# Optimization experiments

Hardware: AMD Instinct MI355X
Metric: run time of the kernel (lower is better)

## Reference

```python
import jax, jax.numpy as jnp
import numpy as np

NX, NY = 512, 512
FNUM, GNUM = 120, 120
NA = 1.35
WAVELENGTH = NX * NA / 100.0  # chosen so normalized period = 100
N_LIQUID = 1.44
M_RED = 0.25
LOW_LIGHT_THRES = 1e-3
SRC_STEEP = 8.0
RESIST_STEEP = 30.0
RESIST_INT = 0.225
DOSES = (0.98, 1.0, 1.02)
SRC_GRID = 13

X1 = NX // 2 - FNUM; X2 = NX // 2 + FNUM + 1
Y1 = NY // 2 - GNUM; Y2 = NY // 2 + GNUM + 1
_PER_X = NX / (WAVELENGTH / NA)
_PER_Y = NY / (WAVELENGTH / NA)
NORM_SPEC = _PER_X * _PER_Y
DFMDG = 1.0 / NORM_SPEC
_fm = (np.arange(X1, X2) - NX // 2) / _PER_X
_gm = (np.arange(Y1, Y2) - NY // 2) / _PER_Y
_FM, _GM = np.meshgrid(_fm, _gm)  # 'xy' indexing, shape [2*GNUM+1, 2*FNUM+1]
FM = jnp.asarray(_FM, jnp.float32)
GM = jnp.asarray(_GM, jnp.float32)


def cal_pupil(fg2):
    # obliquity factor; pupil phase is identically zero in this module
    num = 1.0 - (M_RED ** 2) * (NA ** 2) * fg2
    den = 1.0 - (NA / N_LIQUID) ** 2 * fg2
    return jnp.sqrt(jnp.sqrt(num / den))


def setup_inputs() -> dict:
    key = jax.random.key(0)
    g = np.linspace(-1.0, 1.0, SRC_GRID, dtype=np.float32)
    fxg, fyg = np.meshgrid(g, g)
    r = np.sqrt(fxg ** 2 + fyg ** 2)
    data = ((r >= 0.6) & (r <= 0.9)).astype(np.float32)  # annular source
    # sigmoid activation init: +1 where lit, -1 elsewhere (zeros, set 2 where data>0.5, sub 1)
    params = 2.0 * data - 1.0
    mask_value = jax.random.uniform(key, (NY, NX), jnp.float32)
    return {
        "mask_value": mask_value,
        "source_params": jnp.asarray(params, jnp.float32),
        "source_fx": jnp.asarray(fxg.reshape(-1), jnp.float32),
        "source_fy": jnp.asarray(fyg.reshape(-1), jnp.float32),
    }


def _forward(mask_value, source_params, source_fx, source_fy):
    # source activation + low-light pruning (masked_select expressed as zero-weighting)
    val = jax.nn.sigmoid(SRC_STEEP * source_params).reshape(-1)  # [S]
    valid = val >= LOW_LIGHT_THRES
    w = jnp.where(valid, val, 0.0)
    weight = jnp.sum(w)

    # normalization intensity (detached in the original)
    fxy2 = source_fx ** 2 + source_fy ** 2
    obl = cal_pupil(jnp.where(valid, fxy2, 0.0))
    norm_I = jax.lax.stop_gradient(
        N_LIQUID * DFMDG ** 2 * jnp.sum(w * (NORM_SPEC * obl) ** 2) / weight
    )

    # shifted pupil per source point over the mask frequency window
    F = FM[None, :, :] + source_fx[:, None, None]  # [S, Gy, Gx]
    G = GM[None, :, :] + source_fy[:, None, None]
    rho2 = F * F + G * G                            # == mask_fg2m + 2(fx*fm+fy*gm) + fxy2
    vmask = rho2 <= 1.0
    pupil = jnp.where(vmask, cal_pupil(jnp.where(vmask, rho2, 0.0)), 0.0)  # [S, Gy, Gx]

    S = w.shape[0]
    Is, Rs = [], []
    for d in DOSES:
        fv = jnp.fft.fftshift(jnp.fft.fft2(jnp.fft.ifftshift(mask_value * d)))
        win = fv[Y1:Y2, X1:X2]                      # [Gy, Gx] complex
        tempH = win[None, :, :] * pupil.astype(jnp.complex64)  # masked spectrum*pupil
        e = jnp.zeros((S, NY, NX), jnp.complex64).at[:, Y1:Y2, X1:X2].set(tempH)
        AA = jnp.fft.fftshift(jnp.fft.ifft2(e), axes=(-2, -1))
        I2 = AA.real ** 2 + AA.imag ** 2            # |AA * conj(AA)|
        intensity = jnp.einsum('s,syx->yx', w, I2) / weight / norm_I
        Is.append(intensity)
        Rs.append(jax.nn.sigmoid(RESIST_STEEP * (intensity - RESIST_INT)))
    # [2, 3, NY, NX]: [0] = aerial intensity per dose, [1] = resist image per dose
    return jnp.stack([jnp.stack(Is), jnp.stack(Rs)])


def reference(mask_value, source_params, source_fx, source_fy):
    return _forward(mask_value, source_params, source_fx, source_fy)
```

## Files before the change

kernel.cpp:

```cpp
#include <hip/hip_runtime.h>
#include <hip/hip_bf16.h>
#include <hip/hip_fp16.h>


#define SPLIT 8

static const size_t O_ACC  = 8192;
static const size_t ACC_BYTES = (size_t)SPLIT * 512 * 512 * 4;
static const size_t O_WIN  = O_ACC + ACC_BYTES;
static const size_t O_R1   = O_WIN + 464896;
static const size_t O_T2   = O_R1 + 987136;
static const size_t SLOT_BYTES = (size_t)512 * 244 * 4;

__device__ inline float2 cadd(float2 a, float2 b){ return make_float2(a.x+b.x, a.y+b.y); }
__device__ inline float2 csub(float2 a, float2 b){ return make_float2(a.x-b.x, a.y-b.y); }
__device__ inline float2 cmul(float2 a, float2 b){
  return make_float2(fmaf(a.x, b.x, -(a.y*b.y)), fmaf(a.x, b.y, a.y*b.x));
}
__device__ inline float2 twsgn(float2 t, int S) {
  return make_float2(t.x, (S > 0) ? t.y : -t.y);
}

__device__ inline void build_twt(float2* twt) {
  for (int k = (int)threadIdx.x; k < 512; k += 256) {
    double a = 6.283185307179586476925286766559 * (double)k / 512.0;
    twt[k] = make_float2((float)cos(a), (float)sin(a));
  }
}

template<int S, bool ZTOP>
__device__ inline void dft8(float2 v[8]) {
  const float sg = (float)S;
  const float C7 = 0.7071067811865476f;
  float2 t0, t1, t2, t3, t4, t5, t6, t7;
  if (ZTOP) {
    t0 = v[0]; t4 = v[0];
    t1 = v[1]; t5 = v[1];
    t2 = v[2]; t6 = v[2];
    t3 = v[3]; t7 = v[3];
  } else {
    t0=cadd(v[0],v[4]); t4=csub(v[0],v[4]);
    t1=cadd(v[1],v[5]); t5=csub(v[1],v[5]);
    t2=cadd(v[2],v[6]); t6=csub(v[2],v[6]);
    t3=cadd(v[3],v[7]); t7=csub(v[3],v[7]);
  }
  t5 = make_float2(C7*(t5.x - sg*t5.y), C7*(t5.y + sg*t5.x));
  t6 = make_float2(-sg*t6.y, sg*t6.x);
  t7 = make_float2(C7*(-t7.x - sg*t7.y), C7*(sg*t7.x - t7.y));
  float2 u0=cadd(t0,t2), u2=csub(t0,t2);
  float2 u1=cadd(t1,t3), u3=csub(t1,t3);
  u3 = make_float2(-sg*u3.y, sg*u3.x);
  float2 u4=cadd(t4,t6), u6=csub(t4,t6);
  float2 u5=cadd(t5,t7), u7=csub(t5,t7);
  u7 = make_float2(-sg*u7.y, sg*u7.x);
  v[0]=cadd(u0,u1); v[4]=csub(u0,u1);
  v[2]=cadd(u2,u3); v[6]=csub(u2,u3);
  v[1]=cadd(u4,u5); v[5]=csub(u4,u5);
  v[3]=cadd(u6,u7); v[7]=csub(u6,u7);
}

template<int S, bool ZTOP>
__device__ inline void wfft512(float2 v[8], int lane, float2* xch,
                               const float2* twt) {
  const int p2 = lane & 7, u0 = lane >> 3;
  dft8<S, ZTOP>(v);
  { float2 t1 = twsgn(twt[lane], S), acc = t1;
    v[1] = cmul(v[1], acc);
    #pragma unroll
    for (int u = 2; u < 8; u++) { acc = cmul(acc, t1); v[u] = cmul(v[u], acc); } }
  __builtin_amdgcn_wave_barrier();
  #pragma unroll
  for (int u = 0; u < 8; u++) xch[u*68 + p2*8 + u0] = v[u];
  __builtin_amdgcn_wave_barrier();
  { const float4* rp = (const float4*)(xch + u0*68 + p2*8);
    #pragma unroll
    for (int q = 0; q < 4; q++) {
      float4 t = rp[q];
      v[2*q]   = make_float2(t.x, t.y);
      v[2*q+1] = make_float2(t.z, t.w);
    } }
  dft8<S, false>(v);
  { float2 t1 = twsgn(twt[p2 << 3], S), acc = t1;
    v[1] = cmul(v[1], acc);
    #pragma unroll
    for (int u = 2; u < 8; u++) { acc = cmul(acc, t1); v[u] = cmul(v[u], acc); } }
  __builtin_amdgcn_wave_barrier();
  #pragma unroll
  for (int u = 0; u < 8; u++) xch[u*68 + lane] = v[u];
  __builtin_amdgcn_wave_barrier();
  { const float4* rp = (const float4*)(xch + p2*68 + u0*8);
    #pragma unroll
    for (int q = 0; q < 4; q++) {
      float4 t = rp[q];
      v[2*q]   = make_float2(t.x, t.y);
      v[2*q+1] = make_float2(t.z, t.w);
    } }
  dft8<S, false>(v);
}

__global__ void __launch_bounds__(256, 6) k_b1(const float* mask, const float* prm,
                                               const float* sfx, const float* sfy,
                                               char* ws, float2* R1t) {
  int t = threadIdx.x, lane = t & 63, wv = t >> 6;
  __shared__ __align__(16) float2 lds[4*544];
  __shared__ __align__(16) float2 twt[512];
  build_twt(twt);
  if (blockIdx.x == 0) {
    float*  sw  = (float*)lds;
    float*  sxx = sw + 192; float* syy = sxx + 192; float* scw = syy + 192;
    double* so  = (double*)(sw + 768);
    int*    skp = (int*)(so + 176);
    if (t < 169) {
      float p = prm[t];
      float val = 1.f / (1.f + __expf(-8.f * p));
      float w = (val >= 0.001f) ? val : 0.f;
      double o = 0.0; float fx = 0.f, fy = 0.f;
      if (w > 0.f) {
        fx = sfx[t]; fy = sfy[t];
        double f2 = (double)fx*(double)fx + (double)fy*(double)fy;
        o = (double)w * sqrt((1.0 - 0.11390625 * f2) / (1.0 - 0.87890625 * f2));
      }
      sw[t] = w; so[t] = o; sxx[t] = fx; syy[t] = fy;
    }
    __syncthreads();
    if (t < 169) {
      float w = sw[t];
      int keep = 0; float cw = w;
      if (w > 0.f) {
        float fx = sxx[t], fy = syy[t];
        int pr = -1;
        for (int s2 = 0; s2 < 169; s2++) {
          if (sw[s2] > 0.f && fabsf(sxx[s2] + fx) < 1e-5f
                           && fabsf(syy[s2] + fy) < 1e-5f) { pr = s2; break; }
        }
        if (pr < 0 || pr == t) keep = 1;
        else if (pr > t) { keep = 1; cw = w + sw[pr]; }
      }
      skp[t] = keep; scw[t] = cw;
    }
    __syncthreads();
    if (t == 0) {
      float* wsf = (float*)ws;
      double Sden = 0.0; int c = 0;
      for (int s = 0; s < 169; s++) {
        Sden += so[s];
        if (skp[s]) { wsf[64+c] = scw[s]; wsf[320+c] = sxx[s]; wsf[576+c] = syy[s]; c++; }
      }
      ((int*)ws)[0] = c;
      wsf[1] = (float)(1.0 / (262144.0 * 1.44 * Sden));
    }
  }
  __syncthreads();
  int y = blockIdx.x * 4 + wv;
  float2 v[8];
  #pragma unroll
  for (int q = 0; q < 8; q++) v[q] = make_float2(mask[y*512 + 64*q + lane], 0.f);
  wfft512<-1, false>(v, lane, lds + wv*544, twt);
  #pragma unroll
  for (int u = 0; u < 8; u++) {
    int k = (lane>>3) + 8*(lane&7) + 64*u;
    int beta = (k >= 392) ? (k - 392) : ((k <= 120) ? (k + 120) : -1);
    if (beta >= 0) R1t[beta*512 + y] = v[u];
  }
}

__global__ void __launch_bounds__(256, 6) k_b2(const float2* R1t, float2* Wg) {
  int lane = threadIdx.x & 63, wv = threadIdx.x >> 6;
  int j = blockIdx.x * 4 + wv;
  __shared__ __align__(16) float2 lds[4*544];
  __shared__ __align__(16) float2 twt[512];
  build_twt(twt);
  __syncthreads();
  float2 v[8];
  #pragma unroll
  for (int q = 0; q < 8; q++)
    v[q] = (j < 241) ? R1t[j*512 + 64*q + lane] : make_float2(0.f, 0.f);
  wfft512<-1, false>(v, lane, lds + wv*544, twt);
  if (j < 241) {
    #pragma unroll
    for (int u = 0; u < 8; u++) {
      int k = (lane>>3) + 8*(lane&7) + 64*u;
      int alpha = (k >= 392) ? (k - 392) : ((k <= 120) ? (k + 120) : -1);
      if (alpha >= 0) Wg[alpha*241 + j] = v[u];
    }
  }
}

__global__ void __launch_bounds__(256, 7) k_c1(const float2* Wg, const char* wsb,
                                               int base, int CH, __half2* T2) {
  const float* wsf = (const float*)wsb;
  __shared__ __align__(16) float2 lds[4*544];
  __shared__ __align__(16) float2 twt[512];
  __shared__ float FMt[241];
  build_twt(twt);
  if (threadIdx.x < 241)
    FMt[threadIdx.x] = (float)(((double)((int)threadIdx.x - 120)) / 100.0);
  __syncthreads();
  int active = *(const int*)wsb - base;
  if (active > CH) active = CH;
  int ntask = active * 31;
  int lane = threadIdx.x & 63, wv = threadIdx.x >> 6;
  float2* xch = lds + wv*544;
  for (int task = (int)blockIdx.x; task < ntask; task += (int)gridDim.x) {
    int sic  = task / 31;
    int tile = task % 31;
    int slot = base + sic;
    float fx = wsf[320 + slot], fy = wsf[576 + slot];
    float sqw = __fsqrt_rn(wsf[64 + slot]) * 0.001953125f;
    #pragma unroll
    for (int ph = 0; ph < 2; ph++) {
      int alpha = tile*8 + ph*4 + wv;
      bool arow = (alpha < 241);
      float Gf = __fadd_rn(arow ? FMt[alpha] : 0.f, fy);
      float g2 = __fmul_rn(Gf, Gf);
      bool active_row = arow && (g2 <= 1.0f);
      float2 v[8];
      #pragma unroll
      for (int q = 0; q < 8; q++) v[q] = make_float2(0.f, 0.f);
      if (active_row) {
        #pragma unroll
        for (int q = 0; q < 4; q++) {
          int n = 64*q + lane;
          if (n < 241) {
            float Ff = __fadd_rn(FMt[n], fx);
            float r2 = __fadd_rn(__fmul_rn(Ff, Ff), g2);
            if (r2 <= 1.0f) {
              float num = fmaf(-0.11390625f, r2, 1.0f);
              float den = fmaf(-0.87890625f, r2, 1.0f);
              float P = __fsqrt_rn(__fsqrt_rn(__fdividef(num, den))) * sqw;
              float2 Wv = Wg[alpha*241 + n];
              v[q] = make_float2(P * Wv.x, P * Wv.y);
            }
          }
        }
        wfft512<1, true>(v, lane, xch, twt);
      }
      #pragma unroll
      for (int u = 0; u < 8; u++) {
        int xx = (lane>>3) + 8*(lane&7) + 64*u;
        xch[xx] = v[u];
      }
      __syncthreads();
      int colb = tile*8 + ph*4;
      if (colb < 244) {
        #pragma unroll
        for (int r = 0; r < 2; r++) {
          int x = (int)threadIdx.x + 256*r;
          union { __half2 h[4]; float4 f; } u;
          #pragma unroll
          for (int wvi = 0; wvi < 4; wvi++) {
            float2 a = lds[wvi*544 + x];
            u.h[wvi] = __floats2half2_rn(a.x, a.y);
          }
          *(float4*)(T2 + ((size_t)sic*512 + x)*244 + colb) = u.f;
        }
      }
      __syncthreads();
    }
  }
}

__global__ void __launch_bounds__(256, 7) k_c2(const __half2* T2, const char* wsb,
                                               int base, int CH, int first,
                                               float* accbuf) {
  const int* cnt = (const int*)wsb;
  int part = blockIdx.x & (SPLIT-1);
  int xg   = blockIdx.x >> 3;
  int lane = threadIdx.x & 63, wv = threadIdx.x >> 6;
  int x = xg*4 + wv;
  __shared__ __align__(16) float2 lds[4*544];
  __shared__ __align__(16) float2 twt[512];
  build_twt(twt);
  __syncthreads();
  float2* xch = lds + wv*544;
  int count = *cnt;
  float av[8] = {0.f,0.f,0.f,0.f,0.f,0.f,0.f,0.f};
  int sic = part;
  bool act = (sic < CH) && (base + sic < count);
  __half2 pv[4] = {{0.f,0.f},{0.f,0.f},{0.f,0.f},{0.f,0.f}};
  if (act) {
    const __half2* row = T2 + ((size_t)sic*512 + x)*244;
    #pragma unroll
    for (int q = 0; q < 4; q++) {
      int n = 64*q + lane;
      pv[q] = (n < 241) ? row[n] : __half2{0.f, 0.f};
    }
  }
  while (act) {
    float2 v[8];
    #pragma unroll
    for (int q = 0; q < 4; q++) { float2 f = __half22float2(pv[q]); v[q] = f; }
    #pragma unroll
    for (int q = 4; q < 8; q++) v[q] = make_float2(0.f, 0.f);
    int nsic = sic + SPLIT;
    act = (nsic < CH) && (base + nsic < count);
    if (act) {
      const __half2* row = T2 + ((size_t)nsic*512 + x)*244;
      #pragma unroll
      for (int q = 0; q < 4; q++) {
        int n = 64*q + lane;
        pv[q] = (n < 241) ? row[n] : __half2{0.f, 0.f};
      }
    }
    wfft512<1, true>(v, lane, xch, twt);
    #pragma unroll
    for (int u = 0; u < 8; u++)
      av[u] += fmaf(v[u].x, v[u].x, v[u].y*v[u].y);
    sic = nsic;
  }
  float* a = accbuf + ((size_t)part << 18) + (size_t)x * 512;
  int y0 = (lane>>3) + 8*(lane&7);
  if (first) {
    #pragma unroll
    for (int u = 0; u < 8; u++) a[y0 + 64*u] = av[u];
  } else {
    #pragma unroll
    for (int u = 0; u < 8; u++) a[y0 + 64*u] += av[u];
  }
}

__global__ void __launch_bounds__(256) k_final(const float* acc, const char* wsb,
                                               float* out) {
  __shared__ float tile[64][65];
  const float* wsf = (const float*)wsb;
  float scale = wsf[1];
  int x0 = (blockIdx.x & 7) * 64, y0 = (blockIdx.x >> 3) * 64;
  int j = threadIdx.x & 63, i0 = threadIdx.x >> 6;
  #pragma unroll
  for (int k = 0; k < 16; k++) {
    int i = i0 + 4*k;
    const float* ap = acc + (size_t)(x0 + i)*512 + y0 + j;
    float s = 0.f;
    #pragma unroll
    for (int p = 0; p < SPLIT; p++) s += ap[(size_t)p << 18];
    tile[i][j] = s;
  }
  __syncthreads();
  const float dd[3] = {0.9604f, 1.0f, 1.0404f};
  #pragma unroll
  for (int k = 0; k < 16; k++) {
    int yy = i0 + 4*k;
    float I = scale * tile[j][yy];
    int o = (y0 + yy)*512 + x0 + j;
    #pragma unroll
    for (int d = 0; d < 3; d++) {
      float Ik = dd[d] * I;
      out[(size_t)d*262144 + o] = Ik;
      out[(size_t)(3+d)*262144 + o] = 1.f / (1.f + __expf(-30.f*(Ik - 0.225f)));
    }
  }
}

extern "C" void kernel_launch(void* const* d_in, const int* in_sizes, int n_in,
                              void* d_out, int out_size, void* d_ws, size_t ws_size,
                              hipStream_t stream) {
  (void)in_sizes; (void)n_in; (void)out_size;
  const float* mask = (const float*)d_in[0];
  const float* prm  = (const float*)d_in[1];
  const float* sfx  = (const float*)d_in[2];
  const float* sfy  = (const float*)d_in[3];
  float* out = (float*)d_out;
  char*  ws  = (char*)d_ws;

  float*   acc = (float*)(ws + O_ACC);
  float2*  Wg  = (float2*)(ws + O_WIN);
  float2*  R1t = (float2*)(ws + O_R1);
  __half2* T2  = (__half2*)(ws + O_T2);

  k_b1<<<dim3(128), dim3(256), 0, stream>>>(mask, prm, sfx, sfy, ws, R1t);
  k_b2<<<dim3(61),  dim3(256), 0, stream>>>(R1t, Wg);

  size_t avail = (ws_size > O_T2) ? (ws_size - O_T2) : 0;
  int CH = (int)(avail / SLOT_BYTES);
  if (CH > 169) CH = 169;
  if (CH < 1)   CH = 1;
  for (int base = 0; base < 169; base += CH) {
    k_c1<<<dim3(1024),      dim3(256), 0, stream>>>(Wg, (const char*)ws, base, CH, T2);
    k_c2<<<dim3(128*SPLIT), dim3(256), 0, stream>>>(T2, (const char*)ws, base, CH,
                                                    (base == 0) ? 1 : 0, acc);
  }
  k_final<<<dim3(64), dim3(256), 0, stream>>>(acc, (const char*)ws, out);
}
```

Before: 139.3 us.

## Fuse all pipeline stages into one cooperative persistent kernel with grid syncs

Merges the row FFT, column FFT, pupil-multiply/inverse-FFT stage, accumulation stage and final normalization into a single cooperative kernel. Stages are separated by grid-wide syncs instead of separate launches. The grid is sized from occupancy queries, and the T2 intermediate layout changes to packed 4-column groups. The change targets launch overhead and per-kernel setup such as twiddle table builds, at the cost of grid-sync latency, lower occupancy (launch bounds 4), and idle blocks in small stages.

New measurement: 349.6 us. +151.0%, slower.

```diff
diff --git a/kernel.cpp b/kernel.cpp
--- a/kernel.cpp
+++ b/kernel.cpp
@@ -1,6 +1,8 @@
 #include <hip/hip_runtime.h>
-#include <hip/hip_bf16.h>
 #include <hip/hip_fp16.h>
+#include <hip/hip_cooperative_groups.h>
+
+namespace cg = cooperative_groups;
 
 
 #define SPLIT 8
@@ -98,13 +100,20 @@
   dft8<S, false>(v);
 }
 
-__global__ void __launch_bounds__(256, 6) k_b1(const float* mask, const float* prm,
-                                               const float* sfx, const float* sfy,
-                                               char* ws, float2* R1t) {
-  int t = threadIdx.x, lane = t & 63, wv = t >> 6;
+__global__ void __launch_bounds__(256, 4)
+k_fused(const float* __restrict__ mask, const float* __restrict__ prm,
+        const float* __restrict__ sfx, const float* __restrict__ sfy,
+        char* ws, float2* R1t, float2* Wg, __half2* T2, float* acc,
+        float* out, int CH) {
+  cg::grid_group grid = cg::this_grid();
+  const int t = threadIdx.x, lane = t & 63, wv = t >> 6;
   __shared__ __align__(16) float2 lds[4*544];
   __shared__ __align__(16) float2 twt[512];
+  __shared__ float FMt[241];
   build_twt(twt);
+  if (t < 241) FMt[t] = (float)(((double)(t - 120)) / 100.0);
+  float2* const xch = lds + wv*544;
+
   if (blockIdx.x == 0) {
     float*  sw  = (float*)lds;
     float*  sxx = sw + 192; float* syy = sxx + 192; float* scw = syy + 192;
@@ -140,213 +149,202 @@
     }
     __syncthreads();
     if (t == 0) {
-      float* wsf = (float*)ws;
+      float* wsfw = (float*)ws;
       double Sden = 0.0; int c = 0;
       for (int s = 0; s < 169; s++) {
         Sden += so[s];
-        if (skp[s]) { wsf[64+c] = scw[s]; wsf[320+c] = sxx[s]; wsf[576+c] = syy[s]; c++; }
+        if (skp[s]) { wsfw[64+c] = scw[s]; wsfw[320+c] = sxx[s]; wsfw[576+c] = syy[s]; c++; }
       }
       ((int*)ws)[0] = c;
-      wsf[1] = (float)(1.0 / (262144.0 * 1.44 * Sden));
+      wsfw[1] = (float)(1.0 / (262144.0 * 1.44 * Sden));
     }
   }
   __syncthreads();
-  int y = blockIdx.x * 4 + wv;
-  float2 v[8];
-  #pragma unroll
-  for (int q = 0; q < 8; q++) v[q] = make_float2(mask[y*512 + 64*q + lane], 0.f);
-  wfft512<-1, false>(v, lane, lds + wv*544, twt);
-  #pragma unroll
-  for (int u = 0; u < 8; u++) {
-    int k = (lane>>3) + 8*(lane&7) + 64*u;
-    int beta = (k >= 392) ? (k - 392) : ((k <= 120) ? (k + 120) : -1);
-    if (beta >= 0) R1t[beta*512 + y] = v[u];
-  }
-}
-
-__global__ void __launch_bounds__(256, 6) k_b2(const float2* R1t, float2* Wg) {
-  int lane = threadIdx.x & 63, wv = threadIdx.x >> 6;
-  int j = blockIdx.x * 4 + wv;
-  __shared__ __align__(16) float2 lds[4*544];
-  __shared__ __align__(16) float2 twt[512];
-  build_twt(twt);
-  __syncthreads();
-  float2 v[8];
-  #pragma unroll
-  for (int q = 0; q < 8; q++)
-    v[q] = (j < 241) ? R1t[j*512 + 64*q + lane] : make_float2(0.f, 0.f);
-  wfft512<-1, false>(v, lane, lds + wv*544, twt);
-  if (j < 241) {
+  for (int rb = blockIdx.x; rb < 128; rb += gridDim.x) {
+    int y = rb * 4 + wv;
+    float2 v[8];
+    #pragma unroll
+    for (int q = 0; q < 8; q++) v[q] = make_float2(mask[y*512 + 64*q + lane], 0.f);
+    wfft512<-1, false>(v, lane, xch, twt);
     #pragma unroll
     for (int u = 0; u < 8; u++) {
       int k = (lane>>3) + 8*(lane&7) + 64*u;
-      int alpha = (k >= 392) ? (k - 392) : ((k <= 120) ? (k + 120) : -1);
-      if (alpha >= 0) Wg[alpha*241 + j] = v[u];
-    }
-  }
-}
-
-__global__ void __launch_bounds__(256, 7) k_c1(const float2* Wg, const char* wsb,
-                                               int base, int CH, __half2* T2) {
-  const float* wsf = (const float*)wsb;
-  __shared__ __align__(16) float2 lds[4*544];
-  __shared__ __align__(16) float2 twt[512];
-  __shared__ float FMt[241];
-  build_twt(twt);
-  if (threadIdx.x < 241)
-    FMt[threadIdx.x] = (float)(((double)((int)threadIdx.x - 120)) / 100.0);
-  __syncthreads();
-  int active = *(const int*)wsb - base;
-  if (active > CH) active = CH;
-  int ntask = active * 31;
-  int lane = threadIdx.x & 63, wv = threadIdx.x >> 6;
-  float2* xch = lds + wv*544;
-  for (int task = (int)blockIdx.x; task < ntask; task += (int)gridDim.x) {
-    int sic  = task / 31;
-    int tile = task % 31;
-    int slot = base + sic;
-    float fx = wsf[320 + slot], fy = wsf[576 + slot];
-    float sqw = __fsqrt_rn(wsf[64 + slot]) * 0.001953125f;
-    #pragma unroll
-    for (int ph = 0; ph < 2; ph++) {
-      int alpha = tile*8 + ph*4 + wv;
-      bool arow = (alpha < 241);
-      float Gf = __fadd_rn(arow ? FMt[alpha] : 0.f, fy);
-      float g2 = __fmul_rn(Gf, Gf);
-      bool active_row = arow && (g2 <= 1.0f);
-      float2 v[8];
+      int beta = (k >= 392) ? (k - 392) : ((k <= 120) ? (k + 120) : -1);
+      if (beta >= 0) R1t[beta*512 + y] = v[u];
+    }
+  }
+  grid.sync();
+
+  for (int jb = blockIdx.x; jb < 61; jb += gridDim.x) {
+    int j = jb * 4 + wv;
+    float2 v[8];
+    #pragma unroll
+    for (int q = 0; q < 8; q++)
+      v[q] = (j < 241) ? R1t[j*512 + 64*q + lane] : make_float2(0.f, 0.f);
+    wfft512<-1, false>(v, lane, xch, twt);
+    if (j < 241) {
       #pragma unroll
-      for (int q = 0; q < 8; q++) v[q] = make_float2(0.f, 0.f);
-      if (active_row) {
+      for (int u = 0; u < 8; u++) {
+        int k = (lane>>3) + 8*(lane&7) + 64*u;
+        int alpha = (k >= 392) ? (k - 392) : ((k <= 120) ? (k + 120) : -1);
+        if (alpha >= 0) Wg[alpha*241 + j] = v[u];
+      }
+    }
+  }
+  grid.sync();
+
+  const float* wsf = (const float*)ws;
+  const int count = *(const int*)ws;
+  int nb = (count + CH - 1) / CH;
+  if (nb < 1) nb = 1;
+  for (int bi = 0; bi < nb; bi++) {
+    const int base = bi * CH;
+    int active = count - base;
+    if (active > CH) active = CH;
+    if (active < 0) active = 0;
+    const int ntask = active * 31;
+
+    for (int task = blockIdx.x; task < ntask; task += gridDim.x) {
+      int sic  = task / 31;
+      int tile = task % 31;
+      int slot = base + sic;
+      float fx = wsf[320 + slot], fy = wsf[576 + slot];
+      float sqw = __fsqrt_rn(wsf[64 + slot]) * 0.001953125f;
+      #pragma unroll
+      for (int ph = 0; ph < 2; ph++) {
+        int alpha = tile*8 + ph*4 + wv;
+        bool arow = (alpha < 241);
+        float Gf = __fadd_rn(arow ? FMt[alpha] : 0.f, fy);
+        float g2 = __fmul_rn(Gf, Gf);
+        bool active_row = arow && (g2 <= 1.0f);
+        float2 v[8];
+        #pragma unroll
+        for (int q = 0; q < 8; q++) v[q] = make_float2(0.f, 0.f);
+        if (active_row) {
+          #pragma unroll
+          for (int q = 0; q < 4; q++) {
+            int n = 64*q + lane;
+            if (n < 241) {
+              float Ff = __fadd_rn(FMt[n], fx);
+              float r2 = __fadd_rn(__fmul_rn(Ff, Ff), g2);
+              if (r2 <= 1.0f) {
+                float num = fmaf(-0.11390625f, r2, 1.0f);
+                float den = fmaf(-0.87890625f, r2, 1.0f);
+                float P = __fsqrt_rn(__fsqrt_rn(__fdividef(num, den))) * sqw;
+                float2 Wv = Wg[alpha*241 + n];
+                v[q] = make_float2(P * Wv.x, P * Wv.y);
+              }
+            }
+          }
+          wfft512<1, true>(v, lane, xch, twt);
+        }
+        #pragma unroll
+        for (int u = 0; u < 8; u++) {
+          int xx = (lane>>3) + 8*(lane&7) + 64*u;
+          xch[xx] = v[u];
+        }
+        __syncthreads();
+        int colb = tile*8 + ph*4;
+        if (colb < 244) {
+          #pragma unroll
+          for (int r = 0; r < 2; r++) {
+            int x = t + 256*r;
+            union { __half2 h[4]; float4 f; } uu;
+            #pragma unroll
+            for (int wvi = 0; wvi < 4; wvi++) {
+              float2 a = lds[wvi*544 + x];
+              uu.h[wvi] = __floats2half2_rn(a.x, a.y);
+            }
+            *(float4*)(T2 + ((size_t)(sic*61 + (colb>>2))*512 + x)*4) = uu.f;
+          }
+        }
+        __syncthreads();
+      }
+    }
+    grid.sync();
+
+    for (int unit = blockIdx.x; unit < 1024; unit += gridDim.x) {
+      int part = unit & 7;
+      int x = (unit >> 3) * 4 + wv;
+      float av[8] = {0.f,0.f,0.f,0.f,0.f,0.f,0.f,0.f};
+      int sic = part;
+      bool act = (sic < CH) && (base + sic < count);
+      __half2 pv[4] = {{0.f,0.f},{0.f,0.f},{0.f,0.f},{0.f,0.f}};
+      if (act) {
+        const __half2* sp = T2 + (size_t)sic * (61*512*4);
         #pragma unroll
         for (int q = 0; q < 4; q++) {
           int n = 64*q + lane;
-          if (n < 241) {
-            float Ff = __fadd_rn(FMt[n], fx);
-            float r2 = __fadd_rn(__fmul_rn(Ff, Ff), g2);
-            if (r2 <= 1.0f) {
-              float num = fmaf(-0.11390625f, r2, 1.0f);
-              float den = fmaf(-0.87890625f, r2, 1.0f);
-              float P = __fsqrt_rn(__fsqrt_rn(__fdividef(num, den))) * sqw;
-              float2 Wv = Wg[alpha*241 + n];
-              v[q] = make_float2(P * Wv.x, P * Wv.y);
-            }
+          pv[q] = (n < 241) ? sp[((size_t)(n>>2)*512 + x)*4 + (n&3)]
+                            : __half2{0.f, 0.f};
+        }
+      }
+      while (act) {
+        float2 v[8];
+        #pragma unroll
+        for (int q = 0; q < 4; q++) v[q] = __half22float2(pv[q]);
+        #pragma unroll
+        for (int q = 4; q < 8; q++) v[q] = make_float2(0.f, 0.f);
+        int nsic = sic + SPLIT;
+        act = (nsic < CH) && (base + nsic < count);
+        if (act) {
+          const __half2* sp = T2 + (size_t)nsic * (61*512*4);
+          #pragma unroll
+          for (int q = 0; q < 4; q++) {
+            int n = 64*q + lane;
+            pv[q] = (n < 241) ? sp[((size_t)(n>>2)*512 + x)*4 + (n&3)]
+                              : __half2{0.f, 0.f};
           }
         }
         wfft512<1, true>(v, lane, xch, twt);
-      }
+        #pragma unroll
+        for (int u = 0; u < 8; u++)
+          av[u] += fmaf(v[u].x, v[u].x, v[u].y*v[u].y);
+        sic = nsic;
+      }
+      float* a = acc + ((size_t)part << 18) + (size_t)x * 512;
+      int y0 = (lane>>3) + 8*(lane&7);
+      if (bi == 0) {
+        #pragma unroll
+        for (int u = 0; u < 8; u++) a[y0 + 64*u] = av[u];
+      } else {
+        #pragma unroll
+        for (int u = 0; u < 8; u++) a[y0 + 64*u] += av[u];
+      }
+    }
+    grid.sync();
+  }
+
+  {
+    float scale = wsf[1];
+    float (*tile2)[33] = reinterpret_cast<float(*)[33]>((float*)lds);
+    const float dd[3] = {0.9604f, 1.0f, 1.0404f};
+    int tx = t & 31, ty0 = t >> 5;
+    for (int tb = blockIdx.x; tb < 256; tb += gridDim.x) {
+      int x0 = (tb & 15) * 32, y0 = (tb >> 4) * 32;
       #pragma unroll
-      for (int u = 0; u < 8; u++) {
-        int xx = (lane>>3) + 8*(lane&7) + 64*u;
-        xch[xx] = v[u];
+      for (int r = 0; r < 4; r++) {
+        int i = ty0 + 8*r;
+        const float* ap = acc + (size_t)(x0 + i)*512 + y0 + tx;
+        float s = 0.f;
+        #pragma unroll
+        for (int p = 0; p < SPLIT; p++) s += ap[(size_t)p << 18];
+        tile2[i][tx] = s;
       }
       __syncthreads();
-      int colb = tile*8 + ph*4;
-      if (colb < 244) {
-        #pragma unroll
-        for (int r = 0; r < 2; r++) {
-          int x = (int)threadIdx.x + 256*r;
-          union { __half2 h[4]; float4 f; } u;
-          #pragma unroll
-          for (int wvi = 0; wvi < 4; wvi++) {
-            float2 a = lds[wvi*544 + x];
-            u.h[wvi] = __floats2half2_rn(a.x, a.y);
-          }
-          *(float4*)(T2 + ((size_t)sic*512 + x)*244 + colb) = u.f;
+      #pragma unroll
+      for (int r = 0; r < 4; r++) {
+        int yy = ty0 + 8*r;
+        float I = scale * tile2[tx][yy];
+        int o = (y0 + yy)*512 + x0 + tx;
+        #pragma unroll
+        for (int d = 0; d < 3; d++) {
+          float Ik = dd[d] * I;
+          out[(size_t)d*262144 + o] = Ik;
+          out[(size_t)(3+d)*262144 + o] = 1.f / (1.f + __expf(-30.f*(Ik - 0.225f)));
         }
       }
       __syncthreads();
-    }
-  }
-}
-
-__global__ void __launch_bounds__(256, 7) k_c2(const __half2* T2, const char* wsb,
-                                               int base, int CH, int first,
-                                               float* accbuf) {
-  const int* cnt = (const int*)wsb;
-  int part = blockIdx.x & (SPLIT-1);
-  int xg   = blockIdx.x >> 3;
-  int lane = threadIdx.x & 63, wv = threadIdx.x >> 6;
-  int x = xg*4 + wv;
-  __shared__ __align__(16) float2 lds[4*544];
-  __shared__ __align__(16) float2 twt[512];
-  build_twt(twt);
-  __syncthreads();
-  float2* xch = lds + wv*544;
-  int count = *cnt;
-  float av[8] = {0.f,0.f,0.f,0.f,0.f,0.f,0.f,0.f};
-  int sic = part;
-  bool act = (sic < CH) && (base + sic < count);
-  __half2 pv[4] = {{0.f,0.f},{0.f,0.f},{0.f,0.f},{0.f,0.f}};
-  if (act) {
-    const __half2* row = T2 + ((size_t)sic*512 + x)*244;
-    #pragma unroll
-    for (int q = 0; q < 4; q++) {
-      int n = 64*q + lane;
-      pv[q] = (n < 241) ? row[n] : __half2{0.f, 0.f};
-    }
-  }
-  while (act) {
-    float2 v[8];
-    #pragma unroll
-    for (int q = 0; q < 4; q++) { float2 f = __half22float2(pv[q]); v[q] = f; }
-    #pragma unroll
-    for (int q = 4; q < 8; q++) v[q] = make_float2(0.f, 0.f);
-    int nsic = sic + SPLIT;
-    act = (nsic < CH) && (base + nsic < count);
-    if (act) {
-      const __half2* row = T2 + ((size_t)nsic*512 + x)*244;
-      #pragma unroll
-      for (int q = 0; q < 4; q++) {
-        int n = 64*q + lane;
-        pv[q] = (n < 241) ? row[n] : __half2{0.f, 0.f};
-      }
-    }
-    wfft512<1, true>(v, lane, xch, twt);
-    #pragma unroll
-    for (int u = 0; u < 8; u++)
-      av[u] += fmaf(v[u].x, v[u].x, v[u].y*v[u].y);
-    sic = nsic;
-  }
-  float* a = accbuf + ((size_t)part << 18) + (size_t)x * 512;
-  int y0 = (lane>>3) + 8*(lane&7);
-  if (first) {
-    #pragma unroll
-    for (int u = 0; u < 8; u++) a[y0 + 64*u] = av[u];
-  } else {
-    #pragma unroll
-    for (int u = 0; u < 8; u++) a[y0 + 64*u] += av[u];
-  }
-}
-
-__global__ void __launch_bounds__(256) k_final(const float* acc, const char* wsb,
-                                               float* out) {
-  __shared__ float tile[64][65];
-  const float* wsf = (const float*)wsb;
-  float scale = wsf[1];
-  int x0 = (blockIdx.x & 7) * 64, y0 = (blockIdx.x >> 3) * 64;
-  int j = threadIdx.x & 63, i0 = threadIdx.x >> 6;
-  #pragma unroll
-  for (int k = 0; k < 16; k++) {
-    int i = i0 + 4*k;
-    const float* ap = acc + (size_t)(x0 + i)*512 + y0 + j;
-    float s = 0.f;
-    #pragma unroll
-    for (int p = 0; p < SPLIT; p++) s += ap[(size_t)p << 18];
-    tile[i][j] = s;
-  }
-  __syncthreads();
-  const float dd[3] = {0.9604f, 1.0f, 1.0404f};
-  #pragma unroll
-  for (int k = 0; k < 16; k++) {
-    int yy = i0 + 4*k;
-    float I = scale * tile[j][yy];
-    int o = (y0 + yy)*512 + x0 + j;
-    #pragma unroll
-    for (int d = 0; d < 3; d++) {
-      float Ik = dd[d] * I;
-      out[(size_t)d*262144 + o] = Ik;
-      out[(size_t)(3+d)*262144 + o] = 1.f / (1.f + __expf(-30.f*(Ik - 0.225f)));
     }
   }
 }
@@ -367,17 +365,33 @@
   float2*  R1t = (float2*)(ws + O_R1);
   __half2* T2  = (__half2*)(ws + O_T2);
 
-  k_b1<<<dim3(128), dim3(256), 0, stream>>>(mask, prm, sfx, sfy, ws, R1t);
-  k_b2<<<dim3(61),  dim3(256), 0, stream>>>(R1t, Wg);
-
   size_t avail = (ws_size > O_T2) ? (ws_size - O_T2) : 0;
   int CH = (int)(avail / SLOT_BYTES);
   if (CH > 169) CH = 169;
   if (CH < 1)   CH = 1;
-  for (int base = 0; base < 169; base += CH) {
-    k_c1<<<dim3(1024),      dim3(256), 0, stream>>>(Wg, (const char*)ws, base, CH, T2);
-    k_c2<<<dim3(128*SPLIT), dim3(256), 0, stream>>>(T2, (const char*)ws, base, CH,
-                                                    (base == 0) ? 1 : 0, acc);
-  }
-  k_final<<<dim3(64), dim3(256), 0, stream>>>(acc, (const char*)ws, out);
-}
+
+  static int grid_blocks = 0;
+  if (grid_blocks == 0) {
+    int nbk = 0;
+    if (hipOccupancyMaxActiveBlocksPerMultiprocessor(
+            &nbk, (const void*)k_fused, 256, 0) != hipSuccess || nbk < 1)
+      nbk = 1;
+    int ncu = 256;
+    hipDeviceProp_t prop;
+    int dev = 0;
+    if (hipGetDevice(&dev) == hipSuccess &&
+        hipGetDeviceProperties(&prop, dev) == hipSuccess &&
+        prop.multiProcessorCount > 0)
+      ncu = prop.multiProcessorCount;
+    long g = (long)nbk * (long)ncu;
+    if (g > 1024) g = 1024;
+    if (g < 1) g = 1;
+    grid_blocks = (int)g;
+  }
+
+  void* args[] = { (void*)&mask, (void*)&prm, (void*)&sfx, (void*)&sfy,
+                   (void*)&ws, (void*)&R1t, (void*)&Wg, (void*)&T2,
+                   (void*)&acc, (void*)&out, (void*)&CH };
+  hipLaunchCooperativeKernel((const void*)k_fused, dim3(grid_blocks), dim3(256),
+                             args, 0, stream);
+}
```
